# Optimization experiments

Measured on AMD Instinct MI355X. Metric: run time of the kernel, lower is better.

## Reference

```python
import jax, jax.numpy as jnp
import numpy as np

NEG = -1e16  # matches torch masked_fill value
LN_EPS = 1e-5


def _gat_layer(h, mask, b):
    """h: [..., N, D]; mask: broadcastable bool [..., N, N]; b: broadcastable [..., D]."""
    scores = jnp.einsum('...nd,...md->...nm', h, h)
    scores = jnp.where(mask, scores, NEG)
    attn = jax.nn.softmax(scores, axis=-1)
    return jnp.einsum('...nm,...md->...nd', attn, h) + b


def setup_inputs() -> dict:
    key = jax.random.key(0)
    ks = jax.random.split(key, 6)
    B, N, C, H, D = 8, 2048, 64, 4, 64
    x = jax.random.normal(ks[0], (B, N, C), dtype=jnp.float32)
    graph = jax.random.randint(ks[1], (N, N), 0, 2, dtype=jnp.int32)
    # xavier_uniform-style scale for W: bound = sqrt(6/(fan_in+fan_out))
    bnd_h = float(np.sqrt(6.0 / (C + D)))
    Wh = jax.random.uniform(ks[2], (H, D, C), jnp.float32, -bnd_h, bnd_h)
    bh = jnp.zeros((H, D), jnp.float32)
    bnd_o = float(np.sqrt(6.0 / (H * D + D)))
    Wo = jax.random.uniform(ks[3], (D, H * D), jnp.float32, -bnd_o, bnd_o)
    bo = jnp.zeros((D,), jnp.float32)
    gamma = jnp.ones((D,), jnp.float32)
    beta = jnp.zeros((D,), jnp.float32)
    return {"x": x, "graph": graph, "Wh": Wh, "bh": bh, "Wo": Wo,
            "bo": bo, "gamma": gamma, "beta": beta}


def reference(x, graph, Wh, bh, Wo, bo, gamma, beta):
    B, N, C = x.shape
    H, D, _ = Wh.shape
    # graph = (graph + I) > 0
    mask = (graph + jnp.eye(N, dtype=graph.dtype)) > 0  # [N, N] bool
    # per-head linear projection: [B, H, N, D]
    h = jnp.einsum('bnc,hdc->bhnd', x, Wh)
    out_h = _gat_layer(h, mask[None, None], bh[None, :, None, :])  # [B,H,N,D]
    # torch.cat over heads along last dim == head-major reshape
    cat = jnp.transpose(out_h, (0, 2, 1, 3)).reshape(B, N, H * D)
    z = jax.nn.leaky_relu(cat, negative_slope=0.2)
    h2 = jnp.einsum('bnk,dk->bnd', z, Wo)  # [B, N, D]
    out2 = _gat_layer(h2, mask[None], bo)
    z2 = jax.nn.leaky_relu(out2, negative_slope=0.2)
    # LayerNorm over last dim
    mu = jnp.mean(z2, axis=-1, keepdims=True)
    var = jnp.mean(jnp.square(z2 - mu), axis=-1, keepdims=True)
    out = (z2 - mu) * jax.lax.rsqrt(var + LN_EPS) * gamma + beta
    return out  # dropout p=0.0 -> identity
```

## Files before the change

kernel.cpp:

```cpp
#include <hip/hip_runtime.h>

#define NN 2048
#define PITCH 72
#define MPITCH 264

typedef __attribute__((ext_vector_type(8))) _Float16 half8;
typedef __attribute__((ext_vector_type(4))) float floatx4;

static_assert(sizeof(half8) == 16, "");

#define MRINIT -3.0e38f

__device__ __forceinline__ unsigned short f2h(float f) {
    union { _Float16 h; unsigned short u; } v;
    v.h = (_Float16)f;
    return v.u;
}
__device__ __forceinline__ float h2f(unsigned short u) {
    union { unsigned short u; _Float16 h; } v;
    v.u = u;
    return (float)v.h;
}
__device__ __forceinline__ unsigned int pk2h(float a, float b) {
    union { __fp16 __attribute__((ext_vector_type(2))) h; unsigned int u; } v;
    v.h = __builtin_amdgcn_cvt_pkrtz(a, b);
    return v.u;
}
__device__ __forceinline__ void barrier_lds_only() {
    __asm__ __volatile__("" ::: "memory");
    __builtin_amdgcn_s_waitcnt(0xC07F);
    __builtin_amdgcn_s_barrier();
    __asm__ __volatile__("" ::: "memory");
}

__global__ __launch_bounds__(256) void mask_kernel(const int* __restrict__ graph,
                                                   unsigned int* __restrict__ mbits) {
    const int t = threadIdx.x;
    const int lane = t & 63;
    const int W = (blockIdx.x << 2) + (t >> 6);
    const int i = W >> 5;
    const int cb = W & 31;
    const int j = (cb << 6) + lane;
    const int g = graph[(size_t)i * NN + j];
    const unsigned long long bal = __ballot((g > 0) || (i == j));
    if (lane == 0)  mbits[(i << 6) + (cb << 1)]     = (unsigned int)bal;
    if (lane == 32) mbits[(i << 6) + (cb << 1) + 1] = (unsigned int)(bal >> 32);
}

__global__ __launch_bounds__(256) void proj_gemm(const float* __restrict__ x,
                                                 const float* __restrict__ Wh,
                                                 unsigned short* __restrict__ hout) {
    __shared__ unsigned short xs[64 * PITCH];
    __shared__ unsigned short wh[4 * 64 * PITCH];
    const int t = threadIdx.x;
    const int b = blockIdx.x >> 5;
    const int n0 = (blockIdx.x & 31) << 6;
    for (int i = t; i < 512; i += 256) {
        const int r = i >> 3, c8 = (i & 7) << 3;
        const float* xp = x + (((size_t)b * NN + n0 + r) << 6) + c8;
        const float4 f0 = *(const float4*)(xp);
        const float4 f1 = *(const float4*)(xp + 4);
        uint4 pk;
        pk.x = pk2h(f0.x, f0.y); pk.y = pk2h(f0.z, f0.w);
        pk.z = pk2h(f1.x, f1.y); pk.w = pk2h(f1.z, f1.w);
        *(uint4*)(&xs[r * PITCH + c8]) = pk;
    }
    for (int i = t; i < 2048; i += 256) {
        const int hd = i >> 3, c8 = (i & 7) << 3;
        const float* wp = Wh + ((size_t)hd << 6) + c8;
        const float4 f0 = *(const float4*)(wp);
        const float4 f1 = *(const float4*)(wp + 4);
        uint4 pk;
        pk.x = pk2h(f0.x, f0.y); pk.y = pk2h(f0.z, f0.w);
        pk.z = pk2h(f1.x, f1.y); pk.w = pk2h(f1.z, f1.w);
        *(uint4*)(&wh[hd * PITCH + c8]) = pk;
    }
    __syncthreads();
    const int wave = t >> 6;
    const int m = t & 15;
    const int quad = (t >> 4) & 3;
    half8 bf0[4], bf1[4];
#pragma unroll
    for (int nt = 0; nt < 4; ++nt) {
        const int row = (wave << 6) + (nt << 4) + m;
        bf0[nt] = *(const half8*)(&wh[row * PITCH + (quad << 3)]);
        bf1[nt] = *(const half8*)(&wh[row * PITCH + 32 + (quad << 3)]);
    }
    floatx4 acc[4][4];
#pragma unroll
    for (int mt = 0; mt < 4; ++mt)
#pragma unroll
        for (int nt = 0; nt < 4; ++nt) acc[mt][nt] = floatx4{0.f, 0.f, 0.f, 0.f};
#pragma unroll
    for (int mt = 0; mt < 4; ++mt) {
        const half8 a0 = *(const half8*)(&xs[((mt << 4) + m) * PITCH + (quad << 3)]);
        const half8 a1 = *(const half8*)(&xs[((mt << 4) + m) * PITCH + 32 + (quad << 3)]);
#pragma unroll
        for (int nt = 0; nt < 4; ++nt) {
            acc[mt][nt] = __builtin_amdgcn_mfma_f32_16x16x32_f16(a0, bf0[nt], acc[mt][nt], 0, 0, 0);
            acc[mt][nt] = __builtin_amdgcn_mfma_f32_16x16x32_f16(a1, bf1[nt], acc[mt][nt], 0, 0, 0);
        }
    }
    unsigned short* hp = hout + ((((size_t)(b << 2) + wave) * NN + n0) << 6) + m;
#pragma unroll
    for (int mt = 0; mt < 4; ++mt)
#pragma unroll
        for (int reg = 0; reg < 4; ++reg)
#pragma unroll
            for (int nt = 0; nt < 4; ++nt)
                hp[(((mt << 4) + (quad << 2) + reg) << 6) + (nt << 4)] = f2h(acc[mt][nt][reg]);
}

template <int QG, int OUTMODE>
__global__ __launch_bounds__(256) void gat_flash(const unsigned short* __restrict__ Hm,
                                                 const unsigned int* __restrict__ mbits,
                                                 const float* __restrict__ bias,
                                                 const int bias_mod,
                                                 const float* __restrict__ gamma,
                                                 const float* __restrict__ beta,
                                                 void* __restrict__ OutP,
                                                 float2* __restrict__ mlP) {
    __shared__ unsigned short Ks[2][64 * PITCH];
    __shared__ unsigned short Kts[2][64 * PITCH];
    __shared__ unsigned short Ps[4 * QG * 16 * 64];

    const int t = threadIdx.x;
    const int wave = t >> 6;
    const int lane = t & 63;
    const int quad = lane >> 4;
    const int m = lane & 15;

    const int qtbits = (QG == 2) ? 4 : 5;
    const int bid = blockIdx.x;
    const int qt = bid & ((1 << qtbits) - 1);
    const int split = (OUTMODE == 2) ? ((bid >> qtbits) & 1) : 0;
    const int mat = bid >> (qtbits + ((OUTMODE == 2) ? 1 : 0));
    const int q0 = qt << ((QG == 2) ? 7 : 6);
    const int nkt = (OUTMODE == 2) ? 16 : 32;
    const int kt0 = split * nkt;

    const unsigned short* Hb = Hm + ((size_t)mat << 17);
    const int wbase = q0 + wave * (16 * QG);

    const _Float16 LOG2E = (_Float16)1.44269504f;
    half8 bq0[QG], bq1[QG];
    int gq[QG];
#pragma unroll
    for (int g = 0; g < QG; ++g) {
        gq[g] = wbase + (g << 4) + m;
        bq0[g] = *(const half8*)(Hb + (gq[g] << 6) + (quad << 3)) * LOG2E;
        bq1[g] = *(const half8*)(Hb + (gq[g] << 6) + 32 + (quad << 3)) * LOG2E;
    }

    const int boff = (mat % bias_mod) << 6;
    const float bv0 = bias[boff + m];
    const float bv1 = bias[boff + 16 + m];
    const float bv2 = bias[boff + 32 + m];
    const float bv3 = bias[boff + 48 + m];

    const int p = t >> 3;
    const int cc = t & 7;
    const int jch = p >> 2;
    const int jo = (p & 3) << 1;

    float mr[QG], lr[QG];
    floatx4 O[QG][4];
#pragma unroll
    for (int g = 0; g < QG; ++g) {
        mr[g] = MRINIT;
        lr[g] = 0.f;
#pragma unroll
        for (int nt = 0; nt < 4; ++nt) O[g][nt] = floatx4{0.f, 0.f, 0.f, 0.f};
    }

    const int msw = m & 7;
    int psb[QG];
#pragma unroll
    for (int g = 0; g < QG; ++g) psb[g] = (wave * QG + g) * 1024 + (m << 6);

    const unsigned short* kg0 = Hb + (((kt0 << 6) + (p << 1)) << 6) + (cc << 3);
    half8 ra = *(const half8*)(kg0);
    half8 rb = *(const half8*)(kg0 + 64);

    for (int it = 0; it < nkt; ++it) {
        const int kt = kt0 + it;
        unsigned short* KS = Ks[it & 1];
        unsigned short* KT = Kts[it & 1];
        *(half8*)(&KS[(p << 1) * PITCH + (cc << 3)]) = ra;
        *(half8*)(&KS[((p << 1) + 1) * PITCH + (cc << 3)]) = rb;
        union { half8 v; unsigned int u[4]; } kaU, kbU;
        kaU.v = ra;
        kbU.v = rb;
#pragma unroll
        for (int c = 0; c < 4; ++c) {
            const unsigned int ua = kaU.u[c];
            const unsigned int ub = kbU.u[c];
            const unsigned int lo = __builtin_amdgcn_perm(ub, ua, 0x05040100);
            const unsigned int hi = __builtin_amdgcn_perm(ub, ua, 0x07060302);
            const int d0 = (cc << 3) + (c << 1);
            const int pos = (((jch + cc) & 7) << 3) + jo;
            *(unsigned int*)(&KT[d0 * PITCH + pos]) = lo;
            *(unsigned int*)(&KT[(d0 + 1) * PITCH + pos]) = hi;
        }
        const int ktn = kt0 + ((it + 1) & (nkt - 1));
        const unsigned short* kgn = Hb + (((ktn << 6) + (p << 1)) << 6) + (cc << 3);
        ra = *(const half8*)(kgn);
        rb = *(const half8*)(kgn + 64);

        barrier_lds_only();

        floatx4 a[QG][4];
#pragma unroll
        for (int jt = 0; jt < 4; ++jt) {
            const half8 k0 = *(const half8*)(&KS[((jt << 4) + m) * PITCH + (quad << 3)]);
            const half8 k1 = *(const half8*)(&KS[((jt << 4) + m) * PITCH + 32 + (quad << 3)]);
#pragma unroll
            for (int g = 0; g < QG; ++g) {
                floatx4 z = {0.f, 0.f, 0.f, 0.f};
                z = __builtin_amdgcn_mfma_f32_16x16x32_f16(k0, bq0[g], z, 0, 0, 0);
                z = __builtin_amdgcn_mfma_f32_16x16x32_f16(k1, bq1[g], z, 0, 0, 0);
                a[g][jt] = z;
            }
        }

#pragma unroll
        for (int g = 0; g < QG; ++g) {
            const int mrow = gq[g] << 6;
            const unsigned int w0 = mbits[mrow + (kt << 1)];
            const unsigned int w1 = mbits[mrow + (kt << 1) + 1];

            float tmx = MRINIT;
#pragma unroll
            for (int jt = 0; jt < 4; ++jt) {
                const unsigned int wv = (jt < 2) ? w0 : w1;
                const unsigned int bits = (wv >> (((jt & 1) << 4) + (quad << 2))) & 0xFu;
#pragma unroll
                for (int reg = 0; reg < 4; ++reg) {
                    const float v = ((bits >> reg) & 1u) ? a[g][jt][reg] : MRINIT;
                    a[g][jt][reg] = v;
                    tmx = fmaxf(tmx, v);
                }
            }
            tmx = fmaxf(tmx, __shfl_xor(tmx, 16));
            tmx = fmaxf(tmx, __shfl_xor(tmx, 32));
            const float mnew = fmaxf(mr[g], tmx);
            const float alpha = __builtin_amdgcn_exp2f(mr[g] - mnew);
            const bool need = __any(mnew > mr[g]);

            float psum = 0.f;
#pragma unroll
            for (int jt = 0; jt < 4; ++jt) {
                const float p0 = __builtin_amdgcn_exp2f(a[g][jt][0] - mnew);
                const float p1 = __builtin_amdgcn_exp2f(a[g][jt][1] - mnew);
                const float p2 = __builtin_amdgcn_exp2f(a[g][jt][2] - mnew);
                const float p3 = __builtin_amdgcn_exp2f(a[g][jt][3] - mnew);
                psum += (p0 + p1) + (p2 + p3);
                const int ch = (jt << 1) + (quad >> 1);
                *(uint2*)(&Ps[psb[g] + (((ch + msw) & 7) << 3) + ((quad & 1) << 2)]) =
                    make_uint2(pk2h(p0, p1), pk2h(p2, p3));
            }
            psum += __shfl_xor(psum, 16);
            psum += __shfl_xor(psum, 32);
            lr[g] = lr[g] * alpha + psum;
            mr[g] = mnew;

            if (need) {
                const float aO0 = __shfl(alpha, (quad << 2) + 0);
                const float aO1 = __shfl(alpha, (quad << 2) + 1);
                const float aO2 = __shfl(alpha, (quad << 2) + 2);
                const float aO3 = __shfl(alpha, (quad << 2) + 3);
#pragma unroll
                for (int nt = 0; nt < 4; ++nt) {
                    O[g][nt][0] *= aO0;
                    O[g][nt][1] *= aO1;
                    O[g][nt][2] *= aO2;
                    O[g][nt][3] *= aO3;
                }
            }
        }

        __builtin_amdgcn_wave_barrier();
        __asm__ __volatile__("" ::: "memory");

        half8 pa0[QG], pa1[QG];
#pragma unroll
        for (int g = 0; g < QG; ++g) {
            pa0[g] = *(const half8*)(&Ps[psb[g] + (((quad + msw) & 7) << 3)]);
            pa1[g] = *(const half8*)(&Ps[psb[g] + (((4 + quad + msw) & 7) << 3)]);
        }
#pragma unroll
        for (int nt = 0; nt < 4; ++nt) {
            const int d = (nt << 4) + m;
            const int sw = (d >> 3) & 7;
            const half8 v0 = *(const half8*)(&KT[d * PITCH + (((quad + sw) & 7) << 3)]);
            const half8 v1 = *(const half8*)(&KT[d * PITCH + (((4 + quad + sw) & 7) << 3)]);
#pragma unroll
            for (int g = 0; g < QG; ++g) {
                O[g][nt] = __builtin_amdgcn_mfma_f32_16x16x32_f16(pa0[g], v0, O[g][nt], 0, 0, 0);
                O[g][nt] = __builtin_amdgcn_mfma_f32_16x16x32_f16(pa1[g], v1, O[g][nt], 0, 0, 0);
            }
        }
    }

    if (OUTMODE == 2) {
        float* Ob = (float*)OutP +
                    ((((size_t)(split << 3) + mat) * NN + wbase + (quad << 2)) << 6) + m;
#pragma unroll
        for (int reg = 0; reg < 4; ++reg)
#pragma unroll
            for (int nt = 0; nt < 4; ++nt)
                Ob[(reg << 6) + (nt << 4)] = O[0][nt][reg];
        if (lane < 16)
            mlP[((size_t)(split << 3) + mat) * NN + wbase + m] = make_float2(mr[0], lr[0]);
        return;
    }

    float g0, g1, g2, g3, be0, be1, be2, be3;
    if (OUTMODE == 1) {
        g0 = gamma[m]; g1 = gamma[16 + m]; g2 = gamma[32 + m]; g3 = gamma[48 + m];
        be0 = beta[m]; be1 = beta[16 + m]; be2 = beta[32 + m]; be3 = beta[48 + m];
    }
#pragma unroll
    for (int g = 0; g < QG; ++g) {
        const float l0 = 1.f / __shfl(lr[g], (quad << 2) + 0);
        const float l1 = 1.f / __shfl(lr[g], (quad << 2) + 1);
        const float l2 = 1.f / __shfl(lr[g], (quad << 2) + 2);
        const float l3 = 1.f / __shfl(lr[g], (quad << 2) + 3);
        const size_t obase = (((size_t)mat * NN + wbase + (g << 4) + (quad << 2)) << 6) + m;
#pragma unroll
        for (int reg = 0; reg < 4; ++reg) {
            const float li = (reg == 0) ? l0 : (reg == 1) ? l1 : (reg == 2) ? l2 : l3;
            float z0 = O[g][0][reg] * li + bv0;
            float z1 = O[g][1][reg] * li + bv1;
            float z2 = O[g][2][reg] * li + bv2;
            float z3 = O[g][3][reg] * li + bv3;
            z0 = (z0 > 0.f) ? z0 : 0.2f * z0;
            z1 = (z1 > 0.f) ? z1 : 0.2f * z1;
            z2 = (z2 > 0.f) ? z2 : 0.2f * z2;
            z3 = (z3 > 0.f) ? z3 : 0.2f * z3;
            if (OUTMODE == 0) {
                unsigned short* op = (unsigned short*)OutP + obase + ((size_t)reg << 6);
                op[0] = f2h(z0); op[16] = f2h(z1); op[32] = f2h(z2); op[48] = f2h(z3);
            } else {
                float s = ((z0 + z1) + (z2 + z3));
                float sq = ((z0 * z0 + z1 * z1) + (z2 * z2 + z3 * z3));
#pragma unroll
                for (int off = 1; off < 16; off <<= 1) {
                    s += __shfl_xor(s, off);
                    sq += __shfl_xor(sq, off);
                }
                const float mu = s * 0.015625f;
                float var = sq * 0.015625f - mu * mu;
                var = fmaxf(var, 0.f);
                const float rstd = rsqrtf(var + 1e-5f);
                float* op = (float*)OutP + obase + ((size_t)reg << 6);
                op[0]  = (z0 - mu) * rstd * g0 + be0;
                op[16] = (z1 - mu) * rstd * g1 + be1;
                op[32] = (z2 - mu) * rstd * g2 + be2;
                op[48] = (z3 - mu) * rstd * g3 + be3;
            }
        }
    }
}

__global__ __launch_bounds__(256) void mix_gemm(const unsigned short* __restrict__ oh,
                                                const float* __restrict__ Wo,
                                                unsigned short* __restrict__ h2) {
    __shared__ unsigned short zs[64 * MPITCH];
    __shared__ unsigned short wsm[64 * MPITCH];
    const int t = threadIdx.x;
    const int b = blockIdx.x >> 5;
    const int n0 = (blockIdx.x & 31) << 6;
    for (int i = t; i < 2048; i += 256) {
        const int hh = i >> 9;
        const int r = (i >> 3) & 63;
        const int d8 = i & 7;
        const half8 v = *(const half8*)(oh + ((((size_t)b << 2) + hh) * NN + n0 + r) * 64 + (d8 << 3));
        *(half8*)(&zs[r * MPITCH + (hh << 6) + (d8 << 3)]) = v;
    }
    for (int i = t; i < 2048; i += 256) {
        const int d = i >> 5;
        const int k0 = (i & 31) << 3;
        const float4 f0 = *(const float4*)(Wo + (d << 8) + k0);
        const float4 f1 = *(const float4*)(Wo + (d << 8) + k0 + 4);
        uint4 pk;
        pk.x = pk2h(f0.x, f0.y);
        pk.y = pk2h(f0.z, f0.w);
        pk.z = pk2h(f1.x, f1.y);
        pk.w = pk2h(f1.z, f1.w);
        *(uint4*)(&wsm[d * MPITCH + k0]) = pk;
    }
    __syncthreads();
    const int wave = t >> 6;
    const int m = t & 15;
    const int quad = (t >> 4) & 3;
    const int ar = (wave << 4) + m;
    floatx4 acc[4] = {{0.f, 0.f, 0.f, 0.f}, {0.f, 0.f, 0.f, 0.f},
                      {0.f, 0.f, 0.f, 0.f}, {0.f, 0.f, 0.f, 0.f}};
#pragma unroll
    for (int chunk = 0; chunk < 8; ++chunk) {
        const int k0 = chunk << 5;
        const half8 af = *(const half8*)(&zs[ar * MPITCH + k0 + (quad << 3)]);
#pragma unroll
        for (int nt = 0; nt < 4; ++nt) {
            const half8 bf = *(const half8*)(&wsm[((nt << 4) + m) * MPITCH + k0 + (quad << 3)]);
            acc[nt] = __builtin_amdgcn_mfma_f32_16x16x32_f16(af, bf, acc[nt], 0, 0, 0);
        }
    }
    unsigned short* hp = h2 + (((size_t)b * NN + n0 + (wave << 4) + (quad << 2)) << 6) + m;
#pragma unroll
    for (int reg = 0; reg < 4; ++reg)
#pragma unroll
        for (int nt = 0; nt < 4; ++nt)
            hp[(reg << 6) + (nt << 4)] = f2h(acc[nt][reg]);
}

__global__ __launch_bounds__(256) void combine_ln(const float* __restrict__ Opart,
                                                  const float2* __restrict__ ml,
                                                  const float* __restrict__ bo,
                                                  const float* __restrict__ gamma,
                                                  const float* __restrict__ beta,
                                                  float* __restrict__ out) {
    const int t = threadIdx.x;
    const int lane = t & 63;
    const int widx = (blockIdx.x << 2) + (t >> 6);
    const size_t r0 = (size_t)widx;
    const float2 s0 = ml[r0];
    const float2 s1 = ml[(size_t)(NN * 8) + r0];
    const float mm = fmaxf(s0.x, s1.x);
    const float c0 = __builtin_amdgcn_exp2f(s0.x - mm);
    const float c1 = __builtin_amdgcn_exp2f(s1.x - mm);
    const float l = s0.y * c0 + s1.y * c1;
    const float o0 = Opart[(r0 << 6) + lane];
    const float o1 = Opart[(((size_t)(NN * 8) + r0) << 6) + lane];
    float v = (o0 * c0 + o1 * c1) / l + bo[lane];
    v = (v > 0.f) ? v : 0.2f * v;
    float s = v;
    float sq = v * v;
#pragma unroll
    for (int off = 1; off < 64; off <<= 1) {
        s += __shfl_xor(s, off);
        sq += __shfl_xor(sq, off);
    }
    const float mu = s * 0.015625f;
    float var = sq * 0.015625f - mu * mu;
    var = fmaxf(var, 0.f);
    const float rstd = rsqrtf(var + 1e-5f);
    out[(r0 << 6) + lane] = (v - mu) * rstd * gamma[lane] + beta[lane];
}

extern "C" void kernel_launch(void* const* d_in, const int* in_sizes, int n_in,
                              void* d_out, int out_size, void* d_ws, size_t ws_size,
                              hipStream_t stream) {
    const float* x     = (const float*)d_in[0];
    const int*   graph = (const int*)d_in[1];
    const float* Wh    = (const float*)d_in[2];
    const float* bh    = (const float*)d_in[3];
    const float* Wo    = (const float*)d_in[4];
    const float* bo    = (const float*)d_in[5];
    const float* gamma = (const float*)d_in[6];
    const float* beta  = (const float*)d_in[7];
    float* out = (float*)d_out;

    char* ws = (char*)d_ws;
    unsigned int* mbits = (unsigned int*)ws;
    unsigned short* h   = (unsigned short*)(ws + 0x080000);
    unsigned short* oh  = (unsigned short*)(ws + 0x880000);
    unsigned short* h2  = (unsigned short*)(ws + 0x080000);
    float2* ml          = (float2*)(ws + 0x280000);
    float* Opart        = (float*)(ws + 0x880000);

    mask_kernel<<<16384, 256, 0, stream>>>(graph, mbits);
    proj_gemm<<<256, 256, 0, stream>>>(x, Wh, h);
    gat_flash<2, 0><<<512, 256, 0, stream>>>(h, mbits, bh, 4, nullptr, nullptr, oh, nullptr);
    mix_gemm<<<256, 256, 0, stream>>>(oh, Wo, h2);
    gat_flash<1, 2><<<512, 256, 0, stream>>>(h2, mbits, bo, 1, nullptr, nullptr, Opart, ml);
    combine_ln<<<4096, 256, 0, stream>>>(Opart, ml, bo, gamma, beta, out);
}
```

Before: 206.0 us.

## Use 4-way key split with QG=2 in layer-2 flash, fp16 partials, transposed PV MFMA

The second attention layer now processes two 16-row query groups per wave and splits keys four ways instead of two, keeping 512 blocks. Partial outputs are stored as fp16 with packed vector stores, and combine_ln merges four partials. The PV MFMA operands are swapped so each lane holds a full output row, which drops the alpha and l shuffles and allows packed stores. This trades fewer K/V tile reloads per query against more partial traffic in the combine and some precision loss from fp16 partials.

Measured after the change: 198.9 us. 1.04x faster.

```diff
diff --git a/kernel.cpp b/kernel.cpp
--- a/kernel.cpp
+++ b/kernel.cpp
@@ -111,13 +111,11 @@
                 hp[(((mt << 4) + (quad << 2) + reg) << 6) + (nt << 4)] = f2h(acc[mt][nt][reg]);
 }
 
-template <int QG, int OUTMODE>
+template <int QG, int OUTMODE, int NSPLIT>
 __global__ __launch_bounds__(256) void gat_flash(const unsigned short* __restrict__ Hm,
                                                  const unsigned int* __restrict__ mbits,
                                                  const float* __restrict__ bias,
                                                  const int bias_mod,
-                                                 const float* __restrict__ gamma,
-                                                 const float* __restrict__ beta,
                                                  void* __restrict__ OutP,
                                                  float2* __restrict__ mlP) {
     __shared__ unsigned short Ks[2][64 * PITCH];
@@ -130,13 +128,14 @@
     const int quad = lane >> 4;
     const int m = lane & 15;
 
-    const int qtbits = (QG == 2) ? 4 : 5;
+    const int qtbits = 4;
+    const int sbits = (NSPLIT == 4) ? 2 : (NSPLIT == 2) ? 1 : 0;
     const int bid = blockIdx.x;
     const int qt = bid & ((1 << qtbits) - 1);
-    const int split = (OUTMODE == 2) ? ((bid >> qtbits) & 1) : 0;
-    const int mat = bid >> (qtbits + ((OUTMODE == 2) ? 1 : 0));
-    const int q0 = qt << ((QG == 2) ? 7 : 6);
-    const int nkt = (OUTMODE == 2) ? 16 : 32;
+    const int split = (bid >> qtbits) & (NSPLIT - 1);
+    const int mat = bid >> (qtbits + sbits);
+    const int q0 = qt << 7;
+    const int nkt = 32 / NSPLIT;
     const int kt0 = split * nkt;
 
     const unsigned short* Hb = Hm + ((size_t)mat << 17);
@@ -151,12 +150,6 @@
         bq0[g] = *(const half8*)(Hb + (gq[g] << 6) + (quad << 3)) * LOG2E;
         bq1[g] = *(const half8*)(Hb + (gq[g] << 6) + 32 + (quad << 3)) * LOG2E;
     }
-
-    const int boff = (mat % bias_mod) << 6;
-    const float bv0 = bias[boff + m];
-    const float bv1 = bias[boff + 16 + m];
-    const float bv2 = bias[boff + 32 + m];
-    const float bv3 = bias[boff + 48 + m];
 
     const int p = t >> 3;
     const int cc = t & 7;
@@ -265,16 +258,12 @@
             mr[g] = mnew;
 
             if (need) {
-                const float aO0 = __shfl(alpha, (quad << 2) + 0);
-                const float aO1 = __shfl(alpha, (quad << 2) + 1);
-                const float aO2 = __shfl(alpha, (quad << 2) + 2);
-                const float aO3 = __shfl(alpha, (quad << 2) + 3);
 #pragma unroll
                 for (int nt = 0; nt < 4; ++nt) {
-                    O[g][nt][0] *= aO0;
-                    O[g][nt][1] *= aO1;
-                    O[g][nt][2] *= aO2;
-                    O[g][nt][3] *= aO3;
+                    O[g][nt][0] *= alpha;
+                    O[g][nt][1] *= alpha;
+                    O[g][nt][2] *= alpha;
+                    O[g][nt][3] *= alpha;
                 }
             }
         }
@@ -296,69 +285,51 @@
             const half8 v1 = *(const half8*)(&KT[d * PITCH + (((4 + quad + sw) & 7) << 3)]);
 #pragma unroll
             for (int g = 0; g < QG; ++g) {
-                O[g][nt] = __builtin_amdgcn_mfma_f32_16x16x32_f16(pa0[g], v0, O[g][nt], 0, 0, 0);
-                O[g][nt] = __builtin_amdgcn_mfma_f32_16x16x32_f16(pa1[g], v1, O[g][nt], 0, 0, 0);
+                O[g][nt] = __builtin_amdgcn_mfma_f32_16x16x32_f16(v0, pa0[g], O[g][nt], 0, 0, 0);
+                O[g][nt] = __builtin_amdgcn_mfma_f32_16x16x32_f16(v1, pa1[g], O[g][nt], 0, 0, 0);
             }
         }
     }
 
     if (OUTMODE == 2) {
-        float* Ob = (float*)OutP +
-                    ((((size_t)(split << 3) + mat) * NN + wbase + (quad << 2)) << 6) + m;
-#pragma unroll
-        for (int reg = 0; reg < 4; ++reg)
+        unsigned short* Op = (unsigned short*)OutP;
+        const size_t pbase = ((size_t)(split << 3) + mat) * NN;
+#pragma unroll
+        for (int g = 0; g < QG; ++g) {
+            unsigned short* Ob = Op + ((pbase + gq[g]) << 6) + (quad << 2);
 #pragma unroll
             for (int nt = 0; nt < 4; ++nt)
-                Ob[(reg << 6) + (nt << 4)] = O[0][nt][reg];
-        if (lane < 16)
-            mlP[((size_t)(split << 3) + mat) * NN + wbase + m] = make_float2(mr[0], lr[0]);
+                *(uint2*)(Ob + (nt << 4)) = make_uint2(pk2h(O[g][nt][0], O[g][nt][1]),
+                                                       pk2h(O[g][nt][2], O[g][nt][3]));
+        }
+        if (lane < 16) {
+#pragma unroll
+            for (int g = 0; g < QG; ++g)
+                mlP[pbase + wbase + (g << 4) + m] = make_float2(mr[g], lr[g]);
+        }
         return;
     }
 
-    float g0, g1, g2, g3, be0, be1, be2, be3;
-    if (OUTMODE == 1) {
-        g0 = gamma[m]; g1 = gamma[16 + m]; g2 = gamma[32 + m]; g3 = gamma[48 + m];
-        be0 = beta[m]; be1 = beta[16 + m]; be2 = beta[32 + m]; be3 = beta[48 + m];
-    }
+    const int boff = (mat % bias_mod) << 6;
+    float4 bb[4];
+#pragma unroll
+    for (int nt = 0; nt < 4; ++nt)
+        bb[nt] = *(const float4*)(bias + boff + (nt << 4) + (quad << 2));
 #pragma unroll
     for (int g = 0; g < QG; ++g) {
-        const float l0 = 1.f / __shfl(lr[g], (quad << 2) + 0);
-        const float l1 = 1.f / __shfl(lr[g], (quad << 2) + 1);
-        const float l2 = 1.f / __shfl(lr[g], (quad << 2) + 2);
-        const float l3 = 1.f / __shfl(lr[g], (quad << 2) + 3);
-        const size_t obase = (((size_t)mat * NN + wbase + (g << 4) + (quad << 2)) << 6) + m;
-#pragma unroll
-        for (int reg = 0; reg < 4; ++reg) {
-            const float li = (reg == 0) ? l0 : (reg == 1) ? l1 : (reg == 2) ? l2 : l3;
-            float z0 = O[g][0][reg] * li + bv0;
-            float z1 = O[g][1][reg] * li + bv1;
-            float z2 = O[g][2][reg] * li + bv2;
-            float z3 = O[g][3][reg] * li + bv3;
+        const float li = 1.f / lr[g];
+        unsigned short* op = (unsigned short*)OutP + (((size_t)mat * NN + gq[g]) << 6) + (quad << 2);
+#pragma unroll
+        for (int nt = 0; nt < 4; ++nt) {
+            float z0 = O[g][nt][0] * li + bb[nt].x;
+            float z1 = O[g][nt][1] * li + bb[nt].y;
+            float z2 = O[g][nt][2] * li + bb[nt].z;
+            float z3 = O[g][nt][3] * li + bb[nt].w;
             z0 = (z0 > 0.f) ? z0 : 0.2f * z0;
             z1 = (z1 > 0.f) ? z1 : 0.2f * z1;
             z2 = (z2 > 0.f) ? z2 : 0.2f * z2;
             z3 = (z3 > 0.f) ? z3 : 0.2f * z3;
-            if (OUTMODE == 0) {
-                unsigned short* op = (unsigned short*)OutP + obase + ((size_t)reg << 6);
-                op[0] = f2h(z0); op[16] = f2h(z1); op[32] = f2h(z2); op[48] = f2h(z3);
-            } else {
-                float s = ((z0 + z1) + (z2 + z3));
-                float sq = ((z0 * z0 + z1 * z1) + (z2 * z2 + z3 * z3));
-#pragma unroll
-                for (int off = 1; off < 16; off <<= 1) {
-                    s += __shfl_xor(s, off);
-                    sq += __shfl_xor(sq, off);
-                }
-                const float mu = s * 0.015625f;
-                float var = sq * 0.015625f - mu * mu;
-                var = fmaxf(var, 0.f);
-                const float rstd = rsqrtf(var + 1e-5f);
-                float* op = (float*)OutP + obase + ((size_t)reg << 6);
-                op[0]  = (z0 - mu) * rstd * g0 + be0;
-                op[16] = (z1 - mu) * rstd * g1 + be1;
-                op[32] = (z2 - mu) * rstd * g2 + be2;
-                op[48] = (z3 - mu) * rstd * g3 + be3;
-            }
+            *(uint2*)(op + (nt << 4)) = make_uint2(pk2h(z0, z1), pk2h(z2, z3));
         }
     }
 }
@@ -415,7 +386,7 @@
             hp[(reg << 6) + (nt << 4)] = f2h(acc[nt][reg]);
 }
 
-__global__ __launch_bounds__(256) void combine_ln(const float* __restrict__ Opart,
+__global__ __launch_bounds__(256) void combine_ln(const unsigned short* __restrict__ Opart,
                                                   const float2* __restrict__ ml,
                                                   const float* __restrict__ bo,
                                                   const float* __restrict__ gamma,
@@ -423,17 +394,22 @@
                                                   float* __restrict__ out) {
     const int t = threadIdx.x;
     const int lane = t & 63;
-    const int widx = (blockIdx.x << 2) + (t >> 6);
-    const size_t r0 = (size_t)widx;
-    const float2 s0 = ml[r0];
-    const float2 s1 = ml[(size_t)(NN * 8) + r0];
-    const float mm = fmaxf(s0.x, s1.x);
-    const float c0 = __builtin_amdgcn_exp2f(s0.x - mm);
-    const float c1 = __builtin_amdgcn_exp2f(s1.x - mm);
-    const float l = s0.y * c0 + s1.y * c1;
-    const float o0 = Opart[(r0 << 6) + lane];
-    const float o1 = Opart[(((size_t)(NN * 8) + r0) << 6) + lane];
-    float v = (o0 * c0 + o1 * c1) / l + bo[lane];
+    const size_t r0 = (size_t)((blockIdx.x << 2) + (t >> 6));
+    float2 sv[4];
+    float mm = MRINIT;
+#pragma unroll
+    for (int s = 0; s < 4; ++s) {
+        sv[s] = ml[(size_t)(NN * 8) * s + r0];
+        mm = fmaxf(mm, sv[s].x);
+    }
+    float l = 0.f, osum = 0.f;
+#pragma unroll
+    for (int s = 0; s < 4; ++s) {
+        const float c = __builtin_amdgcn_exp2f(sv[s].x - mm);
+        l += sv[s].y * c;
+        osum += h2f(Opart[(((size_t)(NN * 8) * s + r0) << 6) + lane]) * c;
+    }
+    float v = osum / l + bo[lane];
     v = (v > 0.f) ? v : 0.2f * v;
     float s = v;
     float sq = v * v;
@@ -463,17 +439,17 @@
     float* out = (float*)d_out;
 
     char* ws = (char*)d_ws;
-    unsigned int* mbits = (unsigned int*)ws;
-    unsigned short* h   = (unsigned short*)(ws + 0x080000);
-    unsigned short* oh  = (unsigned short*)(ws + 0x880000);
-    unsigned short* h2  = (unsigned short*)(ws + 0x080000);
-    float2* ml          = (float2*)(ws + 0x280000);
-    float* Opart        = (float*)(ws + 0x880000);
+    unsigned int* mbits   = (unsigned int*)ws;
+    unsigned short* h     = (unsigned short*)(ws + 0x080000);
+    unsigned short* oh    = (unsigned short*)(ws + 0x880000);
+    unsigned short* h2    = (unsigned short*)(ws + 0x080000);
+    float2* ml            = (float2*)(ws + 0x280000);
+    unsigned short* Opart = (unsigned short*)(ws + 0x880000);
 
     mask_kernel<<<16384, 256, 0, stream>>>(graph, mbits);
     proj_gemm<<<256, 256, 0, stream>>>(x, Wh, h);
-    gat_flash<2, 0><<<512, 256, 0, stream>>>(h, mbits, bh, 4, nullptr, nullptr, oh, nullptr);
+    gat_flash<2, 0, 1><<<512, 256, 0, stream>>>(h, mbits, bh, 4, oh, nullptr);
     mix_gemm<<<256, 256, 0, stream>>>(oh, Wo, h2);
-    gat_flash<1, 2><<<512, 256, 0, stream>>>(h2, mbits, bo, 1, nullptr, nullptr, Opart, ml);
+    gat_flash<2, 2, 4><<<512, 256, 0, stream>>>(h2, mbits, bo, 1, Opart, ml);
     combine_ln<<<4096, 256, 0, stream>>>(Opart, ml, bo, gamma, beta, out);
 }
```
